# Kernel tuning notes

Hardware: AMD Instinct MI355X
Metric: run time of the kernel (lower is better)

## Reference

```python
import jax, jax.numpy as jnp
import numpy as np

S, B, D, H, DFF = 1024, 8, 1024, 16, 4096
HD = D // H
EPS = 1e-5


def layernorm(x, g, b):
    m = jnp.mean(x, axis=-1, keepdims=True)
    v = jnp.mean(jnp.square(x - m), axis=-1, keepdims=True)
    return (x - m) * jax.lax.rsqrt(v + EPS) * g + b


def setup_inputs() -> dict:
    key = jax.random.key(0)
    ks = jax.random.split(key, 6)
    w = 0.02
    return {
        "src": jax.random.normal(ks[0], (S, B, D), dtype=jnp.float32),
        "in_proj_w": jax.random.normal(ks[1], (3 * D, D), dtype=jnp.float32) * w,
        "in_proj_b": jnp.zeros((3 * D,), dtype=jnp.float32),
        "out_w": jax.random.normal(ks[2], (D, D), dtype=jnp.float32) * w,
        "out_b": jnp.zeros((D,), dtype=jnp.float32),
        "lin1_w": jax.random.normal(ks[3], (DFF, D), dtype=jnp.float32) * w,
        "lin1_b": jnp.zeros((DFF,), dtype=jnp.float32),
        "lin2_w": jax.random.normal(ks[4], (D, DFF), dtype=jnp.float32) * w,
        "lin2_b": jnp.zeros((D,), dtype=jnp.float32),
        "n1_g": jnp.ones((D,), dtype=jnp.float32),
        "n1_b": jnp.zeros((D,), dtype=jnp.float32),
        "n2_g": jnp.ones((D,), dtype=jnp.float32),
        "n2_b": jnp.zeros((D,), dtype=jnp.float32),
    }


def reference(src, in_proj_w, in_proj_b, out_w, out_b,
              lin1_w, lin1_b, lin2_w, lin2_b,
              n1_g, n1_b, n2_g, n2_b):
    # self-attention block (eval mode: dropout = identity)
    qkv = jnp.einsum('sbd,ed->sbe', src, in_proj_w) + in_proj_b  # [S,B,3D]
    q, k, v = jnp.split(qkv, 3, axis=-1)
    q = q.reshape(S, B, H, HD) * (1.0 / np.sqrt(HD)).astype(np.float32)
    k = k.reshape(S, B, H, HD)
    v = v.reshape(S, B, H, HD)
    scores = jnp.einsum('sbhd,tbhd->bhst', q, k)        # [B,H,S,S]
    attn = jax.nn.softmax(scores, axis=-1)
    o = jnp.einsum('bhst,tbhd->sbhd', attn, v).reshape(S, B, D)
    o = jnp.einsum('sbd,ed->sbe', o, out_w) + out_b
    # post-LN residuals
    x = layernorm(src + o, n1_g, n1_b)
    h = jax.nn.relu(jnp.einsum('sbd,fd->sbf', x, lin1_w) + lin1_b)
    f = jnp.einsum('sbf,df->sbd', h, lin2_w) + lin2_b
    return layernorm(x + f, n2_g, n2_b)
```

## Files before the change

### kernel.cpp

```cpp
#include <hip/hip_runtime.h>
#include <cstdint>
#include <cstddef>

#define S_  1024
#define B_  8
#define D_  1024
#define H_  16
#define HD_ 64
#define DFF_ 4096
#define M_  (S_*B_)
#define QKV_N (3*D_)

typedef float f32x4 __attribute__((ext_vector_type(4)));
typedef __bf16 bf16x8 __attribute__((ext_vector_type(8)));
typedef __bf16 bf16x4 __attribute__((ext_vector_type(4)));

#define GLDS16(gp, lp) __builtin_amdgcn_global_load_lds( \
    (__attribute__((address_space(1))) void*)(gp), \
    (__attribute__((address_space(3))) void*)(lp), 16, 0, 0)

#define CB0 (M_*D_/4)
#define CB1 (CB0 + QKV_N*D_/4)
#define CB2 (CB1 + D_*D_/4)
#define CB3 (CB2 + DFF_*D_/4)
#define CB4 (CB3 + D_*DFF_/4)

__global__ __launch_bounds__(256)
void cvt_all(const float* __restrict__ src, const float* __restrict__ w1f,
             const float* __restrict__ w2f, const float* __restrict__ w3f,
             const float* __restrict__ w4f,
             __bf16* __restrict__ src_bf, __bf16* __restrict__ w1,
             __bf16* __restrict__ w2, __bf16* __restrict__ w3,
             __bf16* __restrict__ w4)
{
    int i = blockIdx.x * 256 + threadIdx.x;
    const float* in; __bf16* out; int off;
    if      (i < CB0) { in = src; out = src_bf; off = 0;   }
    else if (i < CB1) { in = w1f; out = w1;     off = CB0; }
    else if (i < CB2) { in = w2f; out = w2;     off = CB1; }
    else if (i < CB3) { in = w3f; out = w3;     off = CB2; }
    else if (i < CB4) { in = w4f; out = w4;     off = CB3; }
    else return;
    int j = i - off;
    float4 v = *(const float4*)(in + (size_t)j * 4);
    __bf16 t[4] = {(__bf16)v.x, (__bf16)v.y, (__bf16)v.z, (__bf16)v.w};
    *(uint2*)(out + (size_t)j * 4) = *(uint2*)t;
}

template<bool OUT_BF16, bool RELU, bool ADD_BIAS, bool SPLITZ>
__global__ __launch_bounds__(512, 2)
void gemm256(const __bf16* __restrict__ A, const __bf16* __restrict__ W,
             const float* __restrict__ bias,
             void* __restrict__ Cv0, void* __restrict__ Cv1,
             int N, int Kloop, int lda)
{
    extern __shared__ __bf16 lds[];
    __bf16* As = lds;
    __bf16* Bs = lds + 3 * 8192;

    const int tid  = threadIdx.x;
    const int lane = tid & 63;
    const int wv   = tid >> 6;
    const int quad = lane >> 4;
    const int l15  = lane & 15;
    const int wm   = (wv >> 2) * 128;
    const int wn   = (wv & 3) * 64;

    const int id  = blockIdx.y * gridDim.x + blockIdx.x;
    const int nwg = gridDim.x * gridDim.y;
    const int q8  = nwg >> 3;
    const int k   = (id & 7) * q8 + (id >> 3);
    const int within = k & 31;
    const int chunk  = k >> 5;
    const int nchm   = gridDim.x >> 3;
    const int cm     = chunk % nchm;
    const int cn     = chunk / nchm;
    const int m0 = (cm * 8 + (within & 7)) * 256;
    const int n0 = (cn * 4 + (within >> 3)) * 256;

    void* Cv = Cv0;
    if (SPLITZ) {
        const int koff = blockIdx.z * Kloop;
        A += koff;
        W += koff;
        if (blockIdx.z) Cv = Cv1;
    }

    const int nt = Kloop >> 5;

    #define STAGE(kt, buf) do { \
        const int k0s = (kt) << 5; \
        _Pragma("unroll") \
        for (int u = 0; u < 2; ++u) { \
            int c   = u * 512 + tid; \
            int row = c >> 2; \
            int ssl = (c & 3) ^ ((row >> 1) & 3); \
            GLDS16(A + (size_t)(m0 + row) * lda + k0s + ssl * 8, \
                   (char*)(As + (buf) * 8192) + c * 16); \
            GLDS16(W + (size_t)(n0 + row) * lda + k0s + ssl * 8, \
                   (char*)(Bs + (buf) * 8192) + c * 16); \
        } \
    } while (0)

    STAGE(0, 0);
    STAGE(1, 1);
    asm volatile("s_waitcnt vmcnt(4)" ::: "memory");
    __builtin_amdgcn_s_barrier();
    __builtin_amdgcn_sched_barrier(0);

    f32x4 acc[8][4] = {};

    int cur = 0, stg = 2;
    for (int t = 0; t < nt; ++t) {
        if (t + 2 < nt) STAGE(t + 2, stg);

        bf16x8 bf[4], af[8];
        #pragma unroll
        for (int j = 0; j < 4; ++j) {
            int rb = wn + j * 16 + l15;
            bf[j] = *(const bf16x8*)(Bs + cur * 8192 + rb * 32 + (quad ^ ((rb >> 1) & 3)) * 8);
        }
        #pragma unroll
        for (int i = 0; i < 8; ++i) {
            int ra = wm + i * 16 + l15;
            af[i] = *(const bf16x8*)(As + cur * 8192 + ra * 32 + (quad ^ ((ra >> 1) & 3)) * 8);
        }

        __builtin_amdgcn_s_setprio(1);
        #pragma unroll
        for (int i = 0; i < 8; ++i)
            #pragma unroll
            for (int j = 0; j < 4; ++j)
                acc[i][j] = __builtin_amdgcn_mfma_f32_16x16x32_bf16(af[i], bf[j], acc[i][j], 0, 0, 0);
        __builtin_amdgcn_s_setprio(0);

        if (t + 1 < nt) {
            if (t + 2 < nt) { asm volatile("s_waitcnt vmcnt(4)" ::: "memory"); }
            else            { asm volatile("s_waitcnt vmcnt(0)" ::: "memory"); }
            __builtin_amdgcn_s_barrier();
            __builtin_amdgcn_sched_barrier(0);
        }
        if (++cur == 3) cur = 0;
        if (++stg == 3) stg = 0;
    }
    #undef STAGE

    float bvj[4];
    #pragma unroll
    for (int j = 0; j < 4; ++j)
        bvj[j] = ADD_BIAS ? bias[n0 + wn + j * 16 + l15] : 0.f;
    #pragma unroll
    for (int i = 0; i < 8; ++i) {
        const int rbase = m0 + wm + i * 16 + quad * 4;
        #pragma unroll
        for (int r = 0; r < 4; ++r) {
            #pragma unroll
            for (int j = 0; j < 4; ++j) {
                const int col = n0 + wn + j * 16 + l15;
                float v = acc[i][j][r] + bvj[j];
                if (RELU) v = fmaxf(v, 0.f);
                if (OUT_BF16)
                    ((__bf16*)Cv)[(size_t)(rbase + r) * N + col] = (__bf16)v;
                else
                    ((float*)Cv)[(size_t)(rbase + r) * N + col] = v;
            }
        }
    }
}

__global__ __launch_bounds__(256)
void v_transpose(const __bf16* __restrict__ qkv, __bf16* __restrict__ vt)
{
    __shared__ __bf16 T[64 * 65];
    const int tid = threadIdx.x;
    const int t0  = blockIdx.x * 64;
    const int bh  = blockIdx.y;
    const int b   = bh & (B_ - 1);
    const int h   = bh / B_;

    #pragma unroll
    for (int j = 0; j < 2; ++j) {
        int c = j * 256 + tid;
        int i = c >> 3, cc = c & 7;
        const __bf16* g = qkv + (size_t)((t0 + i) * B_ + b) * QKV_N + 2 * D_ + h * HD_ + cc * 8;
        bf16x8 v = *(const bf16x8*)g;
        #pragma unroll
        for (int u = 0; u < 8; ++u) T[(cc * 8 + u) * 65 + i] = v[u];
    }
    __syncthreads();
    #pragma unroll
    for (int j = 0; j < 2; ++j) {
        int c = j * 256 + tid;
        int d = c >> 3, cc = c & 7;
        __bf16 pk[8];
        #pragma unroll
        for (int u = 0; u < 8; ++u) pk[u] = T[d * 65 + cc * 8 + u];
        *(uint4*)(vt + ((size_t)bh * HD_ + d) * S_ + t0 + cc * 8) = *(uint4*)pk;
    }
}

#define AST 64

__global__ __launch_bounds__(512, 6)
void attn_flash(const __bf16* __restrict__ qkv, const __bf16* __restrict__ vt,
                __bf16* __restrict__ out)
{
    __shared__ __bf16 Ks[2][64 * AST];
    __shared__ __bf16 Vs[2][64 * AST];
    __shared__ __bf16 Ps[128 * AST];

    const int tid  = threadIdx.x;
    const int lane = tid & 63;
    const int wv   = tid >> 6;
    const int quad = lane >> 4;
    const int l15  = lane & 15;

    const int id = blockIdx.y * gridDim.x + blockIdx.x;
    const int k  = (id & 7) * ((S_ / 128) * B_ * H_ / 8) + (id >> 3);
    const int s0 = (k & 7) * 128;
    const int bh = k >> 3;
    const int b  = bh & (B_ - 1);
    const int h  = bh / B_;

    {
        int i = tid >> 3, cc = tid & 7;
        int scc = cc ^ (i & 7);
        GLDS16(qkv + (size_t)(i * B_ + b) * QKV_N + D_ + h * HD_ + scc * 8,
               (char*)(Ks[0]) + tid * 16);
        GLDS16(vt + ((size_t)bh * HD_ + i) * S_ + scc * 8,
               (char*)(Vs[0]) + tid * 16);
    }

    const int qrow = wv * 16 + l15;
    bf16x8 bq[2];
    #pragma unroll
    for (int kk = 0; kk < 2; ++kk)
        bq[kk] = *(const bf16x8*)(qkv + (size_t)((s0 + qrow) * B_ + b) * QKV_N
                                  + h * HD_ + kk * 32 + quad * 8);

    __syncthreads();

    f32x4 oacc[4] = {};
    float m_run = -1e30f, l_run = 0.f;
    const float C2    = 0.125f * 1.44269504f;
    const float LOG2E = 1.44269504f;

    const int nt = S_ / 64;
    for (int it = 0; it < nt; ++it) {
        const int cur = it & 1;

        if (it + 1 < nt) {
            const int t1 = (it + 1) * 64;
            int i = tid >> 3, cc = tid & 7;
            int scc = cc ^ (i & 7);
            GLDS16(qkv + (size_t)((t1 + i) * B_ + b) * QKV_N + D_ + h * HD_ + scc * 8,
                   (char*)(Ks[cur ^ 1]) + tid * 16);
            GLDS16(vt + ((size_t)bh * HD_ + i) * S_ + t1 + scc * 8,
                   (char*)(Vs[cur ^ 1]) + tid * 16);
        }

        f32x4 sacc[4] = {};
        #pragma unroll
        for (int kk = 0; kk < 2; ++kk) {
            #pragma unroll
            for (int j = 0; j < 4; ++j) {
                int krow = j * 16 + l15;
                bf16x8 ak = *(const bf16x8*)(&Ks[cur][krow * AST + (((kk * 4 + quad) ^ (krow & 7)) * 8)]);
                sacc[j] = __builtin_amdgcn_mfma_f32_16x16x32_bf16(ak, bq[kk], sacc[j], 0, 0, 0);
            }
        }

        float mx = sacc[0][0];
        #pragma unroll
        for (int j = 0; j < 4; ++j)
            #pragma unroll
            for (int r = 0; r < 4; ++r) mx = fmaxf(mx, sacc[j][r]);
        mx = fmaxf(mx, __shfl_xor(mx, 16, 64));
        mx = fmaxf(mx, __shfl_xor(mx, 32, 64));
        float pm = mx * 0.125f;

        if (!__all(pm - m_run <= 8.0f)) {
            float mnew  = fmaxf(m_run, pm);
            float alpha = __builtin_amdgcn_exp2f((m_run - mnew) * LOG2E);
            l_run *= alpha;
            #pragma unroll
            for (int r = 0; r < 4; ++r) {
                float ar = __shfl(alpha, quad * 4 + r, 64);
                #pragma unroll
                for (int jd = 0; jd < 4; ++jd) oacc[jd][r] *= ar;
            }
            m_run = mnew;
        }

        float k1 = m_run * LOG2E;
        float rs = 0.f;
        #pragma unroll
        for (int j = 0; j < 4; ++j)
            #pragma unroll
            for (int r = 0; r < 4; ++r) {
                float p = __builtin_amdgcn_exp2f(sacc[j][r] * C2 - k1);
                sacc[j][r] = p;
                rs += p;
            }
        rs += __shfl_xor(rs, 16, 64);
        rs += __shfl_xor(rs, 32, 64);
        l_run += rs;

        #pragma unroll
        for (int j = 0; j < 4; ++j) {
            __bf16 pk[4] = {(__bf16)sacc[j][0], (__bf16)sacc[j][1],
                            (__bf16)sacc[j][2], (__bf16)sacc[j][3]};
            int s16 = (j * 2 + (quad >> 1)) ^ (qrow & 7);
            *(uint2*)(Ps + qrow * AST + s16 * 8 + (quad & 1) * 4) = *(uint2*)pk;
        }

        #pragma unroll
        for (int kk = 0; kk < 2; ++kk) {
            bf16x8 ap = *(const bf16x8*)(Ps + qrow * AST + (((kk * 4 + quad) ^ (qrow & 7)) * 8));
            #pragma unroll
            for (int jd = 0; jd < 4; ++jd) {
                int vrow = jd * 16 + l15;
                bf16x8 bv = *(const bf16x8*)(&Vs[cur][vrow * AST + (((kk * 4 + quad) ^ (vrow & 7)) * 8)]);
                oacc[jd] = __builtin_amdgcn_mfma_f32_16x16x32_bf16(ap, bv, oacc[jd], 0, 0, 0);
            }
        }

        __syncthreads();
    }

    float linv = 1.f / l_run;
    #pragma unroll
    for (int r = 0; r < 4; ++r) {
        float lr = __shfl(linv, quad * 4 + r, 64);
        int s = s0 + wv * 16 + quad * 4 + r;
        #pragma unroll
        for (int jd = 0; jd < 4; ++jd) {
            int d = jd * 16 + l15;
            out[(size_t)(s * B_ + b) * D_ + h * HD_ + d] = (__bf16)(oacc[jd][r] * lr);
        }
    }
}

__global__ __launch_bounds__(256)
void ln_res3(const float* __restrict__ xa, const __bf16* __restrict__ p0,
             const __bf16* __restrict__ p1, const float* __restrict__ bias,
             const float* __restrict__ g, const float* __restrict__ beta,
             float* __restrict__ yout, __bf16* __restrict__ ybf)
{
    __shared__ float red[8];
    const int row = blockIdx.x;
    const int tid = threadIdx.x;
    const size_t base = (size_t)row * D_ + tid * 4;

    float4 a  = *(const float4*)(xa + base);
    bf16x4 q0 = *(const bf16x4*)(p0 + base);
    bf16x4 q1 = *(const bf16x4*)(p1 + base);
    float4 bb = *(const float4*)(bias + tid * 4);
    float x0 = a.x + (float)q0[0] + (float)q1[0] + bb.x;
    float x1 = a.y + (float)q0[1] + (float)q1[1] + bb.y;
    float x2 = a.z + (float)q0[2] + (float)q1[2] + bb.z;
    float x3 = a.w + (float)q0[3] + (float)q1[3] + bb.w;

    float s  = x0 + x1 + x2 + x3;
    float ss = x0 * x0 + x1 * x1 + x2 * x2 + x3 * x3;
    for (int msk = 1; msk <= 32; msk <<= 1) {
        s  += __shfl_xor(s,  msk, 64);
        ss += __shfl_xor(ss, msk, 64);
    }
    const int wv = tid >> 6;
    if ((tid & 63) == 0) { red[wv] = s; red[4 + wv] = ss; }
    __syncthreads();
    s  = red[0] + red[1] + red[2] + red[3];
    ss = red[4] + red[5] + red[6] + red[7];
    float mean = s * (1.f / D_);
    float var  = ss * (1.f / D_) - mean * mean;
    float rstd = rsqrtf(var + 1e-5f);

    float4 gv = *(const float4*)(g + tid * 4);
    float4 bv = *(const float4*)(beta + tid * 4);
    float y0 = (x0 - mean) * rstd * gv.x + bv.x;
    float y1 = (x1 - mean) * rstd * gv.y + bv.y;
    float y2 = (x2 - mean) * rstd * gv.z + bv.z;
    float y3 = (x3 - mean) * rstd * gv.w + bv.w;
    *(float4*)(yout + base) = make_float4(y0, y1, y2, y3);
    if (ybf) {
        __bf16 t[4] = {(__bf16)y0, (__bf16)y1, (__bf16)y2, (__bf16)y3};
        *(uint2*)(ybf + base) = *(uint2*)t;
    }
}

extern "C" void kernel_launch(void* const* d_in, const int* in_sizes, int n_in,
                              void* d_out, int out_size, void* d_ws, size_t ws_size,
                              hipStream_t stream)
{
    const float* src       = (const float*)d_in[0];
    const float* in_proj_w = (const float*)d_in[1];
    const float* in_proj_b = (const float*)d_in[2];
    const float* out_w     = (const float*)d_in[3];
    const float* out_b     = (const float*)d_in[4];
    const float* lin1_w    = (const float*)d_in[5];
    const float* lin1_b    = (const float*)d_in[6];
    const float* lin2_w    = (const float*)d_in[7];
    const float* lin2_b    = (const float*)d_in[8];
    const float* n1_g = (const float*)d_in[9];
    const float* n1_b = (const float*)d_in[10];
    const float* n2_g = (const float*)d_in[11];
    const float* n2_b = (const float*)d_in[12];

    char* ws = (char*)d_ws;
    size_t off = 0;
    auto alloc = [&](size_t bytes) { char* p = ws + off; off += (bytes + 255) & ~(size_t)255; return p; };

    __bf16* src_bf = (__bf16*)alloc((size_t)M_ * D_ * 2);
    __bf16* w1     = (__bf16*)alloc((size_t)QKV_N * D_ * 2);
    __bf16* w2     = (__bf16*)alloc((size_t)D_ * D_ * 2);
    __bf16* w3     = (__bf16*)alloc((size_t)DFF_ * D_ * 2);
    __bf16* w4     = (__bf16*)alloc((size_t)D_ * DFF_ * 2);
    __bf16* qkv    = (__bf16*)alloc((size_t)M_ * QKV_N * 2);
    char*   h_r    = alloc((size_t)M_ * DFF_ * 2);
    __bf16* xbf    = (__bf16*)alloc((size_t)M_ * D_ * 2);
    float*  xf     = (float*)alloc((size_t)M_ * D_ * 4);
    __bf16* vt     = (__bf16*)alloc((size_t)B_ * H_ * HD_ * S_ * 2);

    const size_t PART = (size_t)M_ * D_;
    __bf16* attn_o = src_bf;
    __bf16* o0 = (__bf16*)h_r;
    __bf16* o1 = o0 + PART;
    __bf16* hbf = (__bf16*)h_r;
    __bf16* f0 = vt;
    __bf16* f1 = xbf;

    const size_t SHM = 3 * 2 * 8192 * sizeof(__bf16);

    cvt_all<<<(CB4 + 255) / 256, 256, 0, stream>>>(
        src, in_proj_w, out_w, lin1_w, lin2_w, src_bf, w1, w2, w3, w4);

    gemm256<true, false, true, false><<<dim3(M_ / 256, QKV_N / 256), 512, SHM, stream>>>(
        src_bf, w1, in_proj_b, qkv, nullptr, QKV_N, D_, D_);

    v_transpose<<<dim3(S_ / 64, B_ * H_), 256, 0, stream>>>(qkv, vt);

    attn_flash<<<dim3(S_ / 128, B_ * H_), 512, 0, stream>>>(qkv, vt, attn_o);

    gemm256<true, false, false, true><<<dim3(M_ / 256, D_ / 256, 2), 512, SHM, stream>>>(
        attn_o, w2, nullptr, o0, o1, D_, D_ / 2, D_);

    ln_res3<<<M_, 256, 0, stream>>>(src, o0, o1, out_b, n1_g, n1_b, xf, xbf);

    gemm256<true, true, true, false><<<dim3(M_ / 256, DFF_ / 256), 512, SHM, stream>>>(
        xbf, w3, lin1_b, hbf, nullptr, DFF_, D_, D_);

    gemm256<true, false, false, true><<<dim3(M_ / 256, D_ / 256, 2), 512, SHM, stream>>>(
        hbf, w4, nullptr, f0, f1, D_, DFF_ / 2, DFF_);

    ln_res3<<<M_, 256, 0, stream>>>(xf, f0, f1, lin2_b, n2_g, n2_b, (float*)d_out, nullptr);
}
```

Before: 465.4 us.

## Restructure GEMM main loop into 64-wide K tiles with four-phase interleaved prefetch

The 256x256 GEMM moves from a triple-buffered 32-wide K pipeline to a double-buffered 64-wide K tile. Each tile is split into four phases that interleave LDS fragment reads, chunked global-to-LDS prefetches of later tiles, and half-sized MFMA groups, with explicit vmcnt waits and barriers between phases. The aim is finer overlap of memory traffic with matrix math and fewer loop iterations. In exchange, LDS grows to 128 KB per block, which may limit blocks per CU, and it adds more barriers per tile.

```diff
diff --git a/kernel.cpp b/kernel.cpp
--- a/kernel.cpp
+++ b/kernel.cpp
@@ -55,8 +55,6 @@
              int N, int Kloop, int lda)
 {
     extern __shared__ __bf16 lds[];
-    __bf16* As = lds;
-    __bf16* Bs = lds + 3 * 8192;
 
     const int tid  = threadIdx.x;
     const int lane = tid & 63;
@@ -86,64 +84,104 @@
         if (blockIdx.z) Cv = Cv1;
     }
 
-    const int nt = Kloop >> 5;
-
-    #define STAGE(kt, buf) do { \
-        const int k0s = (kt) << 5; \
-        _Pragma("unroll") \
-        for (int u = 0; u < 2; ++u) { \
-            int c   = u * 512 + tid; \
-            int row = c >> 2; \
-            int ssl = (c & 3) ^ ((row >> 1) & 3); \
-            GLDS16(A + (size_t)(m0 + row) * lda + k0s + ssl * 8, \
-                   (char*)(As + (buf) * 8192) + c * 16); \
-            GLDS16(W + (size_t)(n0 + row) * lda + k0s + ssl * 8, \
-                   (char*)(Bs + (buf) * 8192) + c * 16); \
-        } \
-    } while (0)
-
-    STAGE(0, 0);
-    STAGE(1, 1);
-    asm volatile("s_waitcnt vmcnt(4)" ::: "memory");
+    const int nt = Kloop >> 6;
+
+    const int crow = tid >> 2;
+    const int csl  = (tid & 3) ^ ((crow >> 1) & 3);
+
+    #define CHA(kv, hh, kt) GLDS16( \
+        A + (size_t)(m0 + (hh) * 128 + crow) * lda + ((kt) << 6) + (kv) * 32 + csl * 8, \
+        (char*)lds + (((kt) & 1) * 65536 + (kv) * 16384 + (hh) * 8192) + tid * 16)
+    #define CHB(kv, hh, kt) GLDS16( \
+        W + (size_t)(n0 + (hh) * 128 + crow) * lda + ((kt) << 6) + (kv) * 32 + csl * 8, \
+        (char*)lds + (((kt) & 1) * 65536 + 32768 + (kv) * 16384 + (hh) * 8192) + tid * 16)
+
+    CHB(0,0,0); CHB(0,1,0); CHA(0,0,0); CHA(0,1,0);
+    CHB(1,0,0); CHB(1,1,0); CHA(1,0,0); CHA(1,1,0);
+    CHB(0,0,1); CHB(0,1,1); CHA(0,0,1); CHA(0,1,1);
+    CHB(1,0,1); CHB(1,1,1);
+    asm volatile("s_waitcnt vmcnt(6)" ::: "memory");
     __builtin_amdgcn_s_barrier();
     __builtin_amdgcn_sched_barrier(0);
 
     f32x4 acc[8][4] = {};
 
-    int cur = 0, stg = 2;
-    for (int t = 0; t < nt; ++t) {
-        if (t + 2 < nt) STAGE(t + 2, stg);
-
-        bf16x8 bf[4], af[8];
-        #pragma unroll
-        for (int j = 0; j < 4; ++j) {
-            int rb = wn + j * 16 + l15;
-            bf[j] = *(const bf16x8*)(Bs + cur * 8192 + rb * 32 + (quad ^ ((rb >> 1) & 3)) * 8);
-        }
-        #pragma unroll
-        for (int i = 0; i < 8; ++i) {
-            int ra = wm + i * 16 + l15;
-            af[i] = *(const bf16x8*)(As + cur * 8192 + ra * 32 + (quad ^ ((ra >> 1) & 3)) * 8);
-        }
-
-        __builtin_amdgcn_s_setprio(1);
-        #pragma unroll
-        for (int i = 0; i < 8; ++i)
-            #pragma unroll
-            for (int j = 0; j < 4; ++j)
-                acc[i][j] = __builtin_amdgcn_mfma_f32_16x16x32_bf16(af[i], bf[j], acc[i][j], 0, 0, 0);
-        __builtin_amdgcn_s_setprio(0);
-
-        if (t + 1 < nt) {
-            if (t + 2 < nt) { asm volatile("s_waitcnt vmcnt(4)" ::: "memory"); }
-            else            { asm volatile("s_waitcnt vmcnt(0)" ::: "memory"); }
-            __builtin_amdgcn_s_barrier();
-            __builtin_amdgcn_sched_barrier(0);
-        }
-        if (++cur == 3) cur = 0;
-        if (++stg == 3) stg = 0;
-    }
-    #undef STAGE
+    #define RD_A(dst, ii, kkp, CUR) { \
+        int ra = wm + (ii) * 16 + l15; \
+        dst = *(const bf16x8*)(lds + (CUR) + (kkp) * 8192 + ra * 32 + ((quad ^ ((ra >> 1) & 3)) * 8)); }
+    #define RD_B(dst, jj, kkp, CUR) { \
+        int rb = wn + (jj) * 16 + l15; \
+        dst = *(const bf16x8*)(lds + (CUR) + 16384 + (kkp) * 8192 + rb * 32 + ((quad ^ ((rb >> 1) & 3)) * 8)); }
+
+    #define PHASE_SYNC() \
+        __builtin_amdgcn_sched_barrier(0); \
+        __builtin_amdgcn_s_barrier(); \
+        asm volatile("s_waitcnt lgkmcnt(0)" ::: "memory"); \
+        __builtin_amdgcn_sched_barrier(0)
+
+    #define KTILE(T, S1, S2, VM1, VM2) do { \
+        const int cur = ((T) & 1) * 32768; \
+        bf16x8 b_[4], a_[4]; \
+         \
+        _Pragma("unroll") for (int j = 0; j < 4; ++j) RD_B(b_[j], j, 0, cur); \
+        _Pragma("unroll") for (int i = 0; i < 4; ++i) RD_A(a_[i], i, 0, cur); \
+        if (S1) { CHA(1,0,(T)+1); CHA(1,1,(T)+1); } \
+        PHASE_SYNC(); \
+        __builtin_amdgcn_s_setprio(1); \
+        _Pragma("unroll") for (int i = 0; i < 4; ++i) \
+            _Pragma("unroll") for (int j = 0; j < 4; ++j) \
+                acc[i][j] = __builtin_amdgcn_mfma_f32_16x16x32_bf16(a_[i], b_[j], acc[i][j], 0, 0, 0); \
+        __builtin_amdgcn_s_setprio(0); \
+        __builtin_amdgcn_sched_barrier(0); \
+        __builtin_amdgcn_s_barrier(); \
+         \
+        _Pragma("unroll") for (int i = 0; i < 4; ++i) RD_A(a_[i], i + 4, 0, cur); \
+        if (S2) { CHB(0,0,(T)+2); CHB(0,1,(T)+2); } \
+        PHASE_SYNC(); \
+        __builtin_amdgcn_s_setprio(1); \
+        _Pragma("unroll") for (int i = 0; i < 4; ++i) \
+            _Pragma("unroll") for (int j = 0; j < 4; ++j) \
+                acc[i+4][j] = __builtin_amdgcn_mfma_f32_16x16x32_bf16(a_[i], b_[j], acc[i+4][j], 0, 0, 0); \
+        __builtin_amdgcn_s_setprio(0); \
+        asm volatile("s_waitcnt vmcnt(" VM1 ")" ::: "memory"); \
+        __builtin_amdgcn_sched_barrier(0); \
+        __builtin_amdgcn_s_barrier(); \
+         \
+        _Pragma("unroll") for (int j = 0; j < 4; ++j) RD_B(b_[j], j, 1, cur); \
+        _Pragma("unroll") for (int i = 0; i < 4; ++i) RD_A(a_[i], i, 1, cur); \
+        if (S2) { CHA(0,0,(T)+2); CHA(0,1,(T)+2); } \
+        PHASE_SYNC(); \
+        __builtin_amdgcn_s_setprio(1); \
+        _Pragma("unroll") for (int i = 0; i < 4; ++i) \
+            _Pragma("unroll") for (int j = 0; j < 4; ++j) \
+                acc[i][j] = __builtin_amdgcn_mfma_f32_16x16x32_bf16(a_[i], b_[j], acc[i][j], 0, 0, 0); \
+        __builtin_amdgcn_s_setprio(0); \
+        __builtin_amdgcn_sched_barrier(0); \
+        __builtin_amdgcn_s_barrier(); \
+         \
+        _Pragma("unroll") for (int i = 0; i < 4; ++i) RD_A(a_[i], i + 4, 1, cur); \
+        if (S2) { CHB(1,0,(T)+2); CHB(1,1,(T)+2); } \
+        PHASE_SYNC(); \
+        __builtin_amdgcn_s_setprio(1); \
+        _Pragma("unroll") for (int i = 0; i < 4; ++i) \
+            _Pragma("unroll") for (int j = 0; j < 4; ++j) \
+                acc[i+4][j] = __builtin_amdgcn_mfma_f32_16x16x32_bf16(a_[i], b_[j], acc[i+4][j], 0, 0, 0); \
+        __builtin_amdgcn_s_setprio(0); \
+        asm volatile("s_waitcnt vmcnt(" VM2 ")" ::: "memory"); \
+        __builtin_amdgcn_sched_barrier(0); \
+        __builtin_amdgcn_s_barrier(); \
+    } while (0)
+
+    for (int t = 0; t < nt - 2; ++t) KTILE(t, true, true, "10", "10");
+    KTILE(nt - 2, true,  false, "8", "4");
+    KTILE(nt - 1, false, false, "0", "0");
+
+    #undef KTILE
+    #undef PHASE_SYNC
+    #undef RD_A
+    #undef RD_B
+    #undef CHA
+    #undef CHB
 
     float bvj[4];
     #pragma unroll
@@ -430,7 +468,7 @@
     __bf16* f0 = vt;
     __bf16* f1 = xbf;
 
-    const size_t SHM = 3 * 2 * 8192 * sizeof(__bf16);
+    const size_t SHM = 131072;
 
     cvt_all<<<(CB4 + 255) / 256, 256, 0, stream>>>(
         src, in_proj_w, out_w, lin1_w, lin2_w, src_bf, w1, w2, w3, w4);
```

Result: no change. 457.9 us (-1.6%).

## Switch GEMM to double-buffered 64-wide K tiles with larger LDS stages

Applied to the files above, without the earlier changes.

The bf16 GEMM's K pipeline changes from a triple-buffered scheme with 32-wide K tiles to a double-buffered scheme with 64-wide K tiles. Each stage now loads twice as much A/W data and runs two MFMA sub-steps per tile, which halves the number of barriers and waits over K. The cost is a shallower prefetch: the loop waits with vmcnt(0) on the single next stage, which can leave more global-load latency exposed. LDS per block grows to 128 KB.

```diff
diff --git a/kernel.cpp b/kernel.cpp
--- a/kernel.cpp
+++ b/kernel.cpp
@@ -55,8 +55,6 @@
              int N, int Kloop, int lda)
 {
     extern __shared__ __bf16 lds[];
-    __bf16* As = lds;
-    __bf16* Bs = lds + 3 * 8192;
 
     const int tid  = threadIdx.x;
     const int lane = tid & 63;
@@ -86,64 +84,68 @@
         if (blockIdx.z) Cv = Cv1;
     }
 
-    const int nt = Kloop >> 5;
+    const int nt = Kloop >> 6;
+
+    const int crow = tid >> 2;
+    const int csl  = (tid & 3) ^ ((crow >> 1) & 3);
+
+    #define CHA(kv, hh, kt, buf) GLDS16( \
+        A + (size_t)(m0 + (hh) * 128 + crow) * lda + ((kt) << 6) + (kv) * 32 + csl * 8, \
+        (char*)lds + ((buf) * 65536 + (kv) * 16384 + (hh) * 8192) + tid * 16)
+    #define CHB(kv, hh, kt, buf) GLDS16( \
+        W + (size_t)(n0 + (hh) * 128 + crow) * lda + ((kt) << 6) + (kv) * 32 + csl * 8, \
+        (char*)lds + ((buf) * 65536 + 32768 + (kv) * 16384 + (hh) * 8192) + tid * 16)
 
     #define STAGE(kt, buf) do { \
-        const int k0s = (kt) << 5; \
-        _Pragma("unroll") \
-        for (int u = 0; u < 2; ++u) { \
-            int c   = u * 512 + tid; \
-            int row = c >> 2; \
-            int ssl = (c & 3) ^ ((row >> 1) & 3); \
-            GLDS16(A + (size_t)(m0 + row) * lda + k0s + ssl * 8, \
-                   (char*)(As + (buf) * 8192) + c * 16); \
-            GLDS16(W + (size_t)(n0 + row) * lda + k0s + ssl * 8, \
-                   (char*)(Bs + (buf) * 8192) + c * 16); \
-        } \
+        CHB(0,0,kt,buf); CHB(0,1,kt,buf); CHA(0,0,kt,buf); CHA(0,1,kt,buf); \
+        CHB(1,0,kt,buf); CHB(1,1,kt,buf); CHA(1,0,kt,buf); CHA(1,1,kt,buf); \
     } while (0)
 
     STAGE(0, 0);
-    STAGE(1, 1);
-    asm volatile("s_waitcnt vmcnt(4)" ::: "memory");
+    asm volatile("s_waitcnt vmcnt(0)" ::: "memory");
     __builtin_amdgcn_s_barrier();
     __builtin_amdgcn_sched_barrier(0);
 
     f32x4 acc[8][4] = {};
 
-    int cur = 0, stg = 2;
     for (int t = 0; t < nt; ++t) {
-        if (t + 2 < nt) STAGE(t + 2, stg);
-
-        bf16x8 bf[4], af[8];
-        #pragma unroll
-        for (int j = 0; j < 4; ++j) {
-            int rb = wn + j * 16 + l15;
-            bf[j] = *(const bf16x8*)(Bs + cur * 8192 + rb * 32 + (quad ^ ((rb >> 1) & 3)) * 8);
-        }
-        #pragma unroll
-        for (int i = 0; i < 8; ++i) {
-            int ra = wm + i * 16 + l15;
-            af[i] = *(const bf16x8*)(As + cur * 8192 + ra * 32 + (quad ^ ((ra >> 1) & 3)) * 8);
-        }
-
-        __builtin_amdgcn_s_setprio(1);
-        #pragma unroll
-        for (int i = 0; i < 8; ++i)
-            #pragma unroll
-            for (int j = 0; j < 4; ++j)
-                acc[i][j] = __builtin_amdgcn_mfma_f32_16x16x32_bf16(af[i], bf[j], acc[i][j], 0, 0, 0);
-        __builtin_amdgcn_s_setprio(0);
+        const int cur = t & 1;
+        if (t + 1 < nt) STAGE(t + 1, cur ^ 1);
+
+        #pragma unroll
+        for (int kk = 0; kk < 2; ++kk) {
+            bf16x8 b_[4], a_[8];
+            #pragma unroll
+            for (int j = 0; j < 4; ++j) {
+                int rb = wn + j * 16 + l15;
+                b_[j] = *(const bf16x8*)(lds + cur * 32768 + 16384 + kk * 8192
+                                         + rb * 32 + ((quad ^ ((rb >> 1) & 3)) * 8));
+            }
+            #pragma unroll
+            for (int i = 0; i < 8; ++i) {
+                int ra = wm + i * 16 + l15;
+                a_[i] = *(const bf16x8*)(lds + cur * 32768 + kk * 8192
+                                         + ra * 32 + ((quad ^ ((ra >> 1) & 3)) * 8));
+            }
+            __builtin_amdgcn_s_setprio(1);
+            #pragma unroll
+            for (int i = 0; i < 8; ++i)
+                #pragma unroll
+                for (int j = 0; j < 4; ++j)
+                    acc[i][j] = __builtin_amdgcn_mfma_f32_16x16x32_bf16(a_[i], b_[j], acc[i][j], 0, 0, 0);
+            __builtin_amdgcn_s_setprio(0);
+        }
 
         if (t + 1 < nt) {
-            if (t + 2 < nt) { asm volatile("s_waitcnt vmcnt(4)" ::: "memory"); }
-            else            { asm volatile("s_waitcnt vmcnt(0)" ::: "memory"); }
+            asm volatile("s_waitcnt vmcnt(0)" ::: "memory");
             __builtin_amdgcn_s_barrier();
             __builtin_amdgcn_sched_barrier(0);
         }
-        if (++cur == 3) cur = 0;
-        if (++stg == 3) stg = 0;
-    }
+    }
+
     #undef STAGE
+    #undef CHA
+    #undef CHB
 
     float bvj[4];
     #pragma unroll
@@ -430,7 +432,7 @@
     __bf16* f0 = vt;
     __bf16* f1 = xbf;
 
-    const size_t SHM = 3 * 2 * 8192 * sizeof(__bf16);
+    const size_t SHM = 131072;
 
     cvt_all<<<(CB4 + 255) / 256, 256, 0, stream>>>(
         src, in_proj_w, out_w, lin1_w, lin2_w, src_bf, w1, w2, w3, w4);
```

Result: no change. 469.6 us (+0.9%).
